# Kernel optimization log

Hardware: AMD Instinct MI355X
Metric: run time of the kernel (lower is better)

The kernel has to match this reference:

```python
import jax, jax.numpy as jnp
import numpy as np

H = 1024      # hidden_size
E = 8         # num_experts
I = 1024      # moe_intermediate_size
SI = 2816     # shared_expert_intermediate_size
B, S = 2, 2048


def setup_inputs() -> dict:
    key = jax.random.key(0)
    ks = jax.random.split(key, 10)
    sc = lambda fan_in: 1.0 / np.sqrt(fan_in)
    return {
        "hidden_states": jax.random.normal(ks[0], (B, S, H), dtype=jnp.float32),
        "gate_w": jax.random.normal(ks[1], (E, H), dtype=jnp.float32) * sc(H),
        "wg": jax.random.normal(ks[2], (E, I, H), dtype=jnp.float32) * sc(H),   # gate_proj per expert
        "wu": jax.random.normal(ks[3], (E, I, H), dtype=jnp.float32) * sc(H),   # up_proj per expert
        "wd": jax.random.normal(ks[4], (E, H, I), dtype=jnp.float32) * sc(I),   # down_proj per expert
        "swg": jax.random.normal(ks[5], (SI, H), dtype=jnp.float32) * sc(H),    # shared gate_proj
        "swu": jax.random.normal(ks[6], (SI, H), dtype=jnp.float32) * sc(H),    # shared up_proj
        "swd": jax.random.normal(ks[7], (H, SI), dtype=jnp.float32) * sc(SI),   # shared down_proj
        "shared_gate_w": jax.random.normal(ks[8], (1, H), dtype=jnp.float32) * sc(H),
        "top_k": 2,
    }


def reference(hidden_states, gate_w, wg, wu, wd, swg, swu, swd, shared_gate_w, top_k):
    b, s, h = hidden_states.shape
    flat = hidden_states.reshape(-1, h)                      # [T,H]
    # router
    logits = flat @ gate_w.T                                 # [T,E]
    probs = jax.nn.softmax(logits, axis=-1)
    vals, idx = jax.lax.top_k(probs, top_k)                  # [T,K]
    vals = vals / jnp.sum(vals, axis=-1, keepdims=True)      # norm_topk_prob
    # combine weights scattered to full expert dim: [T,E]
    combine = jnp.sum(jax.nn.one_hot(idx, E, dtype=flat.dtype) * vals[..., None], axis=1)
    # dense per-expert SwiGLU FFN over all tokens, masked-combined (same math)
    g = jax.nn.silu(jnp.einsum("th,eih->eti", flat, wg))     # [E,T,I]
    u = jnp.einsum("th,eih->eti", flat, wu)
    eo = jnp.einsum("eti,ehi->eth", g * u, wd)               # [E,T,H]
    expert_out = jnp.einsum("te,eth->th", combine, eo)       # [T,H]
    # shared expert with sigmoid gate
    shared = (jax.nn.silu(flat @ swg.T) * (flat @ swu.T)) @ swd.T   # [T,H]
    sgate = jax.nn.sigmoid(flat @ shared_gate_w.T)           # [T,1]
    out = expert_out + sgate * shared
    return out.reshape(b, s, h)
```

## Files before the change

kernel.cpp:

```cpp
#include <hip/hip_runtime.h>
#include <stdint.h>

#define TT  4096
#define HD  1024
#define NE  8
#define ID  1024
#define SID 2816

typedef short s16x8 __attribute__((ext_vector_type(8)));
typedef float f32x4 __attribute__((ext_vector_type(4)));
typedef float f32x4v __attribute__((ext_vector_type(4)));
typedef unsigned short u16x4 __attribute__((ext_vector_type(4)));

__device__ __forceinline__ ushort f2bf(float f) {
  uint32_t u = __float_as_uint(f);
  u += 0x7FFFu + ((u >> 16) & 1u);
  return (ushort)(u >> 16);
}

__device__ __forceinline__ float bf2f(ushort u) {
  return __uint_as_float((uint32_t)u << 16);
}

__device__ __forceinline__ void gll16(const ushort* g, ushort* l) {
  __builtin_amdgcn_global_load_lds(
      (const __attribute__((address_space(1))) void*)g,
      (__attribute__((address_space(3))) void*)l, 16, 0, 0);
}

struct CvtArgs {
  const float* src[6];
  ushort* dst[6];
  int n[6];
};

__global__ __launch_bounds__(256) void cvt_all(CvtArgs a) {
  int t = blockIdx.y;
  int i = (blockIdx.x * 256 + threadIdx.x) * 4;
  if (i >= a.n[t]) return;
  f32x4v v = *(const f32x4v*)(a.src[t] + i);
  u16x4 o;
  o.x = f2bf(v.x); o.y = f2bf(v.y); o.z = f2bf(v.z); o.w = f2bf(v.w);
  *(u16x4*)(a.dst[t] + i) = o;
}

__global__ __launch_bounds__(256) void router_k(
    const float* __restrict__ X, const float* __restrict__ gw,
    const float* __restrict__ sgw, ushort* __restrict__ Xb,
    int* __restrict__ topki, float* __restrict__ topkw,
    float* __restrict__ sgate) {
  __shared__ float gwL[(NE + 1) * HD];
  #pragma unroll
  for (int i = 0; i < NE * HD / 1024; i++) {
    int idx = i * 1024 + threadIdx.x * 4;
    *(f32x4*)&gwL[idx] = *(const f32x4*)&gw[idx];
  }
  {
    int idx = threadIdx.x * 4;
    if (idx < HD) *(f32x4*)&gwL[NE * HD + idx] = *(const f32x4*)&sgw[idx];
  }
  __syncthreads();

  const int wave = threadIdx.x >> 6, lane = threadIdx.x & 63;
  #pragma unroll
  for (int tt = 0; tt < 4; tt++) {
    const int t = blockIdx.x * 16 + wave * 4 + tt;
    const float* x = X + (size_t)t * HD;
    float acc[NE + 1];
    #pragma unroll
    for (int e = 0; e <= NE; e++) acc[e] = 0.f;
    #pragma unroll
    for (int p = 0; p < HD / 256; p++) {
      const int k = p * 256 + lane * 4;
      f32x4 xv = *(const f32x4*)&x[k];
      u16x4 xb;
      xb.x = f2bf(xv.x); xb.y = f2bf(xv.y); xb.z = f2bf(xv.z); xb.w = f2bf(xv.w);
      *(u16x4*)&Xb[(size_t)t * HD + k] = xb;
      #pragma unroll
      for (int e = 0; e < NE; e++) {
        f32x4 g = *(const f32x4*)&gwL[e * HD + k];
        acc[e] += xv.x * g.x + xv.y * g.y + xv.z * g.z + xv.w * g.w;
      }
      f32x4 s = *(const f32x4*)&gwL[NE * HD + k];
      acc[NE] += xv.x * s.x + xv.y * s.y + xv.z * s.z + xv.w * s.w;
    }
    #pragma unroll
    for (int off = 32; off > 0; off >>= 1)
      #pragma unroll
      for (int e = 0; e <= NE; e++)
        acc[e] += __shfl_xor(acc[e], off, 64);
    if (lane == 0) {
      float m = acc[0];
      #pragma unroll
      for (int e = 1; e < NE; e++) m = fmaxf(m, acc[e]);
      float p[NE];
      #pragma unroll
      for (int e = 0; e < NE; e++) p[e] = __expf(acc[e] - m);
      int i1 = 0;
      #pragma unroll
      for (int e = 1; e < NE; e++) if (p[e] > p[i1]) i1 = e;
      int i2 = (i1 == 0) ? 1 : 0;
      #pragma unroll
      for (int e = 0; e < NE; e++) if (e != i1 && p[e] > p[i2]) i2 = e;
      float inv = 1.f / (p[i1] + p[i2]);
      topki[2 * t] = i1; topki[2 * t + 1] = i2;
      topkw[2 * t] = p[i1] * inv; topkw[2 * t + 1] = p[i2] * inv;
      sgate[t] = 1.f / (1.f + __expf(-acc[NE]));
    }
  }
}

__global__ __launch_bounds__(1024) void binning_k(
    const int* __restrict__ topki, const float* __restrict__ topkw,
    int* __restrict__ cnt, int* __restrict__ offs,
    int* __restrict__ tokmap, float* __restrict__ wmap,
    int* __restrict__ smap) {
  __shared__ int wc[16][NE];
  __shared__ int wbase[16][NE];
  const int tid = threadIdx.x;
  const int wave = tid >> 6, lane = tid & 63;
  const uint64_t ltmask = ((uint64_t)1 << lane) - 1;

  int wcnt[NE];
  #pragma unroll
  for (int e = 0; e < NE; e++) wcnt[e] = 0;
  int mye[8], myoff[8];
  #pragma unroll
  for (int it = 0; it < 8; it++) {
    int s = wave * 512 + it * 64 + lane;
    int e = topki[s];
    mye[it] = e;
    myoff[it] = 0;
    #pragma unroll
    for (int ee = 0; ee < NE; ee++) {
      uint64_t m = __ballot(e == ee);
      if (e == ee) myoff[it] = wcnt[ee] + __popcll(m & ltmask);
      wcnt[ee] += __popcll(m);
    }
  }
  if (lane == 0) {
    #pragma unroll
    for (int e = 0; e < NE; e++) wc[wave][e] = wcnt[e];
  }
  __syncthreads();
  if (tid == 0) {
    int o = 0;
    for (int e = 0; e < NE; e++) {
      offs[e] = o;
      int tot = 0;
      for (int w = 0; w < 16; w++) { wbase[w][e] = o + tot; tot += wc[w][e]; }
      cnt[e] = tot;
      o += tot;
    }
  }
  __syncthreads();
  #pragma unroll
  for (int it = 0; it < 8; it++) {
    int s = wave * 512 + it * 64 + lane;
    int e = mye[it];
    int pos = wbase[wave][e] + myoff[it];
    tokmap[pos] = s >> 1;
    wmap[pos] = topkw[s];
    smap[s] = pos;
  }
}

constexpr int BM = 128, BN = 128, BK = 32;

template <bool GATHER>
__device__ __forceinline__ void gu_core(
    const ushort* __restrict__ A, const ushort* __restrict__ Wg,
    const ushort* __restrict__ Wu, ushort* __restrict__ Hout,
    const int* __restrict__ tokmap, int cnt, int seg,
    int mb, int nb, int N, int K) {
  const int m0 = mb * BM;
  if (m0 >= cnt) return;
  const int n0 = nb * BN;

  __shared__ ushort lA[2][BM * BK];
  __shared__ ushort lBg[2][BN * BK];
  __shared__ ushort lBu[2][BN * BK];

  const int tid = threadIdx.x;
  const int wave = tid >> 6, lane = tid & 63;
  const int wm = (wave >> 1) * 64, wn = (wave & 1) * 64;

  const int ar0 = wave * 32 + (lane >> 2);
  const int ar1 = ar0 + 16;
  const int kc = ((lane & 3) ^ ((lane >> 3) & 3)) * 8;

  const ushort *a0p, *a1p;
  if (GATHER) {
    int m_ = m0 + ar0;
    int tk0 = (m_ < cnt) ? tokmap[seg + m_] : 0;
    m_ = m0 + ar1;
    int tk1 = (m_ < cnt) ? tokmap[seg + m_] : 0;
    a0p = A + (size_t)tk0 * K + kc;
    a1p = A + (size_t)tk1 * K + kc;
  } else {
    a0p = A + (size_t)(m0 + ar0) * K + kc;
    a1p = A + (size_t)(m0 + ar1) * K + kc;
  }
  const ushort* bg0 = Wg + (size_t)(n0 + ar0) * K + kc;
  const ushort* bg1 = Wg + (size_t)(n0 + ar1) * K + kc;
  const ushort* bu0 = Wu + (size_t)(n0 + ar0) * K + kc;
  const ushort* bu1 = Wu + (size_t)(n0 + ar1) * K + kc;

  f32x4 accG[4][4], accU[4][4];
  #pragma unroll
  for (int i = 0; i < 4; i++)
    #pragma unroll
    for (int j = 0; j < 4; j++) {
      accG[i][j] = f32x4{0.f, 0.f, 0.f, 0.f};
      accU[i][j] = f32x4{0.f, 0.f, 0.f, 0.f};
    }

  const int lr = lane & 15;
  const int lk = (((lane >> 4) ^ ((lr >> 1) & 3))) * 8;
  const int w32 = wave * 32;

  auto stage = [&](int b, int k0) {
    gll16(a0p + k0, &lA[b][w32 * BK]);
    gll16(a1p + k0, &lA[b][(w32 + 16) * BK]);
    gll16(bg0 + k0, &lBg[b][w32 * BK]);
    gll16(bg1 + k0, &lBg[b][(w32 + 16) * BK]);
    gll16(bu0 + k0, &lBu[b][w32 * BK]);
    gll16(bu1 + k0, &lBu[b][(w32 + 16) * BK]);
  };

  const int nt = K / BK;
  stage(0, 0);
  for (int t = 0; t < nt; t++) {
    const int cur = t & 1;
    if (t + 1 < nt) {
      stage(cur ^ 1, (t + 1) * BK);
      asm volatile("s_waitcnt vmcnt(6)" ::: "memory");
    } else {
      asm volatile("s_waitcnt vmcnt(0)" ::: "memory");
    }
    __builtin_amdgcn_s_barrier();

    s16x8 af[4], bgf[4], buf_[4];
    #pragma unroll
    for (int i = 0; i < 4; i++) {
      af[i]   = *(const s16x8*)&lA [cur][(wm + i * 16 + lr) * BK + lk];
      bgf[i]  = *(const s16x8*)&lBg[cur][(wn + i * 16 + lr) * BK + lk];
      buf_[i] = *(const s16x8*)&lBu[cur][(wn + i * 16 + lr) * BK + lk];
    }
    #pragma unroll
    for (int i = 0; i < 4; i++)
      #pragma unroll
      for (int j = 0; j < 4; j++) {
        accG[i][j] = __builtin_amdgcn_mfma_f32_16x16x32_bf16(af[i], bgf[j], accG[i][j], 0, 0, 0);
        accU[i][j] = __builtin_amdgcn_mfma_f32_16x16x32_bf16(af[i], buf_[j], accU[i][j], 0, 0, 0);
      }
    __builtin_amdgcn_s_barrier();
  }

  const int lrr = (lane >> 4) * 4;
  #pragma unroll
  for (int i = 0; i < 4; i++) {
    #pragma unroll
    for (int r = 0; r < 4; r++) {
      int m = wm + i * 16 + lrr + r;
      if (m0 + m < cnt) {
        size_t row = (size_t)(seg + m0 + m) * N;
        #pragma unroll
        for (int j = 0; j < 4; j++) {
          int c = n0 + wn + j * 16 + lr;
          float g = accG[i][j][r];
          float u = accU[i][j][r];
          float s = g / (1.f + __expf(-g));
          Hout[row + c] = f2bf(s * u);
        }
      }
    }
  }
}

__device__ __forceinline__ void dn_core(
    const ushort* __restrict__ A, const ushort* __restrict__ W,
    ushort* __restrict__ outB, int cnt, int seg,
    int mb, int nb, int N, int K) {
  const int m0 = mb * BM;
  if (m0 >= cnt) return;
  const int n0 = nb * BN;

  __shared__ ushort lA[2][BM * BK];
  __shared__ ushort lB[2][BN * BK];

  const int tid = threadIdx.x;
  const int wave = tid >> 6, lane = tid & 63;
  const int wm = (wave >> 1) * 64, wn = (wave & 1) * 64;

  const int ar0 = wave * 32 + (lane >> 2);
  const int ar1 = ar0 + 16;
  const int kc = ((lane & 3) ^ ((lane >> 3) & 3)) * 8;

  int r0 = m0 + ar0; if (r0 > cnt - 1) r0 = cnt - 1;
  int r1 = m0 + ar1; if (r1 > cnt - 1) r1 = cnt - 1;
  const ushort* a0p = A + (size_t)(seg + r0) * K + kc;
  const ushort* a1p = A + (size_t)(seg + r1) * K + kc;
  const ushort* b0 = W + (size_t)(n0 + ar0) * K + kc;
  const ushort* b1 = W + (size_t)(n0 + ar1) * K + kc;

  f32x4 acc[4][4];
  #pragma unroll
  for (int i = 0; i < 4; i++)
    #pragma unroll
    for (int j = 0; j < 4; j++) acc[i][j] = f32x4{0.f, 0.f, 0.f, 0.f};

  const int lr = lane & 15;
  const int lk = (((lane >> 4) ^ ((lr >> 1) & 3))) * 8;
  const int w32 = wave * 32;

  auto stage = [&](int b, int k0) {
    gll16(a0p + k0, &lA[b][w32 * BK]);
    gll16(a1p + k0, &lA[b][(w32 + 16) * BK]);
    gll16(b0 + k0, &lB[b][w32 * BK]);
    gll16(b1 + k0, &lB[b][(w32 + 16) * BK]);
  };

  const int nt = K / BK;
  stage(0, 0);
  for (int t = 0; t < nt; t++) {
    const int cur = t & 1;
    if (t + 1 < nt) {
      stage(cur ^ 1, (t + 1) * BK);
      asm volatile("s_waitcnt vmcnt(4)" ::: "memory");
    } else {
      asm volatile("s_waitcnt vmcnt(0)" ::: "memory");
    }
    __builtin_amdgcn_s_barrier();

    s16x8 af[4], bf[4];
    #pragma unroll
    for (int i = 0; i < 4; i++) {
      af[i] = *(const s16x8*)&lA[cur][(wm + i * 16 + lr) * BK + lk];
      bf[i] = *(const s16x8*)&lB[cur][(wn + i * 16 + lr) * BK + lk];
    }
    #pragma unroll
    for (int i = 0; i < 4; i++)
      #pragma unroll
      for (int j = 0; j < 4; j++)
        acc[i][j] = __builtin_amdgcn_mfma_f32_16x16x32_bf16(af[i], bf[j], acc[i][j], 0, 0, 0);
    __builtin_amdgcn_s_barrier();
  }

  const int lrr = (lane >> 4) * 4;
  #pragma unroll
  for (int i = 0; i < 4; i++) {
    #pragma unroll
    for (int r = 0; r < 4; r++) {
      int m = wm + i * 16 + lrr + r;
      if (m0 + m < cnt) {
        size_t row = (size_t)(seg + m0 + m) * N;
        #pragma unroll
        for (int j = 0; j < 4; j++) {
          int c = n0 + wn + j * 16 + lr;
          outB[row + c] = f2bf(acc[i][j][r]);
        }
      }
    }
  }
}

__global__ __launch_bounds__(256, 2) void gemm_gu_s(
    const ushort* __restrict__ A, const ushort* __restrict__ Wg,
    const ushort* __restrict__ Wu, ushort* __restrict__ H,
    int M, int N, int K) {
  int id = blockIdx.x;
  int x = id & 7, k = id >> 3;
  int mb = (x & 3) * 8 + (k & 7);
  int nb = (x >> 2) * 11 + (k >> 3);
  gu_core<false>(A, Wg, Wu, H, nullptr, M, 0, mb, nb, N, K);
}

__global__ __launch_bounds__(256, 2) void gemm_gu_r(
    const ushort* __restrict__ A, const ushort* __restrict__ Wg,
    const ushort* __restrict__ Wu, ushort* __restrict__ H,
    const int* __restrict__ tokmap, const int* __restrict__ cnts,
    const int* __restrict__ offs, int N, int K) {
  int e = blockIdx.x;
  gu_core<true>(A, Wg + (size_t)e * N * K, Wu + (size_t)e * N * K, H,
                tokmap, cnts[e], offs[e], blockIdx.y, blockIdx.z, N, K);
}

__global__ __launch_bounds__(256, 2) void gemm_dn_s(
    const ushort* __restrict__ A, const ushort* __restrict__ W,
    float* __restrict__ out, const float* __restrict__ sgate,
    int M, int N, int K) {
  int id = blockIdx.x;
  int x = id & 7, kk = id >> 3;
  int mb = x * 4 + (kk & 3);
  int nb = kk >> 2;
  const int m0 = mb * 128, n0 = nb * 64;

  __shared__ ushort lA[2][128 * 32];
  __shared__ ushort lB[2][64 * 32];

  const int tid = threadIdx.x;
  const int wave = tid >> 6, lane = tid & 63;
  const int wm = (wave >> 1) * 64, wn = (wave & 1) * 32;

  const int ar0 = wave * 32 + (lane >> 2);
  const int ar1 = ar0 + 16;
  const int br  = wave * 16 + (lane >> 2);
  const int kc = ((lane & 3) ^ ((lane >> 3) & 3)) * 8;

  const ushort* a0p = A + (size_t)(m0 + ar0) * K + kc;
  const ushort* a1p = A + (size_t)(m0 + ar1) * K + kc;
  const ushort* bp  = W + (size_t)(n0 + br) * K + kc;

  f32x4 acc[4][2];
  #pragma unroll
  for (int i = 0; i < 4; i++)
    #pragma unroll
    for (int j = 0; j < 2; j++) acc[i][j] = f32x4{0.f, 0.f, 0.f, 0.f};

  const int lr = lane & 15;
  const int lk = (((lane >> 4) ^ ((lr >> 1) & 3))) * 8;
  const int w32 = wave * 32;

  auto stage = [&](int b, int k0) {
    gll16(a0p + k0, &lA[b][w32 * 32]);
    gll16(a1p + k0, &lA[b][(w32 + 16) * 32]);
    gll16(bp + k0, &lB[b][wave * 512]);
  };

  const int nt = K / 32;
  stage(0, 0);
  for (int t = 0; t < nt; t++) {
    const int cur = t & 1;
    if (t + 1 < nt) {
      stage(cur ^ 1, (t + 1) * 32);
      asm volatile("s_waitcnt vmcnt(3)" ::: "memory");
    } else {
      asm volatile("s_waitcnt vmcnt(0)" ::: "memory");
    }
    __builtin_amdgcn_s_barrier();

    s16x8 af[4], bf[2];
    #pragma unroll
    for (int i = 0; i < 4; i++)
      af[i] = *(const s16x8*)&lA[cur][(wm + i * 16 + lr) * 32 + lk];
    #pragma unroll
    for (int j = 0; j < 2; j++)
      bf[j] = *(const s16x8*)&lB[cur][(wn + j * 16 + lr) * 32 + lk];
    #pragma unroll
    for (int i = 0; i < 4; i++)
      #pragma unroll
      for (int j = 0; j < 2; j++)
        acc[i][j] = __builtin_amdgcn_mfma_f32_16x16x32_bf16(af[i], bf[j], acc[i][j], 0, 0, 0);
    __builtin_amdgcn_s_barrier();
  }

  const int lrr = (lane >> 4) * 4;
  #pragma unroll
  for (int i = 0; i < 4; i++) {
    #pragma unroll
    for (int r = 0; r < 4; r++) {
      int m = m0 + wm + i * 16 + lrr + r;
      float wv = sgate[m];
      size_t row = (size_t)m * N;
      #pragma unroll
      for (int j = 0; j < 2; j++) {
        int c = n0 + wn + j * 16 + lr;
        out[row + c] = wv * acc[i][j][r];
      }
    }
  }
}

__global__ __launch_bounds__(256, 2) void gemm_dn_r(
    const ushort* __restrict__ A, const ushort* __restrict__ W,
    ushort* __restrict__ eo, const int* __restrict__ cnts,
    const int* __restrict__ offs, int N, int K) {
  int e = blockIdx.x;
  dn_core(A, W + (size_t)e * N * K, eo, cnts[e], offs[e],
          blockIdx.y, blockIdx.z, N, K);
}

__global__ __launch_bounds__(256) void combine_k(
    const ushort* __restrict__ eo, const float* __restrict__ topkw,
    const int* __restrict__ smap, float* __restrict__ out) {
  int t = blockIdx.x;
  int c = threadIdx.x * 4;
  int s0 = smap[2 * t], s1 = smap[2 * t + 1];
  float w0 = topkw[2 * t], w1 = topkw[2 * t + 1];
  u16x4 a = *(const u16x4*)&eo[(size_t)s0 * HD + c];
  u16x4 b = *(const u16x4*)&eo[(size_t)s1 * HD + c];
  float* o = out + (size_t)t * HD + c;
  f32x4 ov = *(const f32x4*)o;
  #pragma unroll
  for (int j = 0; j < 4; j++)
    ov[j] += w0 * bf2f(a[j]) + w1 * bf2f(b[j]);
  *(f32x4*)o = ov;
}

extern "C" void kernel_launch(void* const* d_in, const int* in_sizes, int n_in,
                              void* d_out, int out_size, void* d_ws, size_t ws_size,
                              hipStream_t stream) {
  const float* hs  = (const float*)d_in[0];
  const float* gw  = (const float*)d_in[1];
  const float* wg  = (const float*)d_in[2];
  const float* wu  = (const float*)d_in[3];
  const float* wd  = (const float*)d_in[4];
  const float* swg = (const float*)d_in[5];
  const float* swu = (const float*)d_in[6];
  const float* swd = (const float*)d_in[7];
  const float* sgw = (const float*)d_in[8];
  float* out = (float*)d_out;

  uint8_t* base = (uint8_t*)d_ws;
  size_t off = 0;
  auto give = [&](size_t b) -> void* {
    void* p = base + off;
    off += (b + 255) & ~(size_t)255;
    return p;
  };
  ushort* Xb   = (ushort*)give((size_t)TT * HD * 2);
  ushort* wgB  = (ushort*)give((size_t)NE * ID * HD * 2);
  ushort* wuB  = (ushort*)give((size_t)NE * ID * HD * 2);
  ushort* wdB  = (ushort*)give((size_t)NE * HD * ID * 2);
  ushort* sgB  = (ushort*)give((size_t)SID * HD * 2);
  ushort* suB  = (ushort*)give((size_t)SID * HD * 2);
  ushort* sdB  = (ushort*)give((size_t)HD * SID * 2);
  ushort* Sbuf = (ushort*)give((size_t)TT * SID * 2);
  ushort* Hbuf = (ushort*)give((size_t)2 * TT * ID * 2);
  float* sgate = (float*)give(TT * 4);
  int* topki   = (int*)give(TT * 2 * 4);
  float* topkw = (float*)give(TT * 2 * 4);
  int* tokmap  = (int*)give(2 * TT * 4);
  float* wmap  = (float*)give(2 * TT * 4);
  int* smap    = (int*)give(2 * TT * 4);
  int* cnt     = (int*)give(256);
  int* offs    = (int*)give(256);

  CvtArgs ca;
  ca.src[0] = wg;  ca.dst[0] = wgB; ca.n[0] = NE * ID * HD;
  ca.src[1] = wu;  ca.dst[1] = wuB; ca.n[1] = NE * ID * HD;
  ca.src[2] = wd;  ca.dst[2] = wdB; ca.n[2] = NE * HD * ID;
  ca.src[3] = swg; ca.dst[3] = sgB; ca.n[3] = SID * HD;
  ca.src[4] = swu; ca.dst[4] = suB; ca.n[4] = SID * HD;
  ca.src[5] = swd; ca.dst[5] = sdB; ca.n[5] = HD * SID;
  cvt_all<<<dim3(8192, 6), 256, 0, stream>>>(ca);

  router_k<<<TT / 16, 256, 0, stream>>>(hs, gw, sgw, Xb, topki, topkw, sgate);
  binning_k<<<1, 1024, 0, stream>>>(topki, topkw, cnt, offs, tokmap, wmap, smap);

  gemm_gu_s<<<(TT / BM) * (SID / BN), 256, 0, stream>>>(
      Xb, sgB, suB, Sbuf, TT, SID, HD);
  gemm_dn_s<<<(TT / 128) * (HD / 64), 256, 0, stream>>>(
      Sbuf, sdB, out, sgate, TT, HD, SID);

  gemm_gu_r<<<dim3(NE, 2 * TT / BM, ID / BN), 256, 0, stream>>>(
      Xb, wgB, wuB, Hbuf, tokmap, cnt, offs, ID, HD);
  gemm_dn_r<<<dim3(NE, 2 * TT / BM, HD / BN), 256, 0, stream>>>(
      Hbuf, wdB, Sbuf , cnt, offs, HD, ID);

  combine_k<<<TT, 256, 0, stream>>>(Sbuf, topkw, smap, out);
}
```

Baseline: 276.4 us.

## Merge shared and routed expert GEMMs into combined launches with atomic combine

Shared-expert and routed-expert gate/up GEMMs now run in one launch, and the two down-projection GEMMs run in another, with blocks split by index. The routed down-projection scatters weighted results straight into the fp32 output with atomicAdd, which removes the bf16 intermediate buffer, the smap table and the separate combine kernel. The shared down-projection also uses atomicAdd, and the output is zeroed with a memset first. This cuts launches and tail idle time and fills the GPU with both workloads at once. In exchange it adds atomic traffic and makes the fp32 summation order nondeterministic. Many routed blocks (64 M-tiles per expert) exit early.

```diff
diff --git a/kernel.cpp b/kernel.cpp
--- a/kernel.cpp
+++ b/kernel.cpp
@@ -113,8 +113,7 @@
 __global__ __launch_bounds__(1024) void binning_k(
     const int* __restrict__ topki, const float* __restrict__ topkw,
     int* __restrict__ cnt, int* __restrict__ offs,
-    int* __restrict__ tokmap, float* __restrict__ wmap,
-    int* __restrict__ smap) {
+    int* __restrict__ tokmap, float* __restrict__ wmap) {
   __shared__ int wc[16][NE];
   __shared__ int wbase[16][NE];
   const int tid = threadIdx.x;
@@ -161,7 +160,6 @@
     int pos = wbase[wave][e] + myoff[it];
     tokmap[pos] = s >> 1;
     wmap[pos] = topkw[s];
-    smap[s] = pos;
   }
 }
 
@@ -172,14 +170,14 @@
     const ushort* __restrict__ A, const ushort* __restrict__ Wg,
     const ushort* __restrict__ Wu, ushort* __restrict__ Hout,
     const int* __restrict__ tokmap, int cnt, int seg,
-    int mb, int nb, int N, int K) {
+    int mb, int nb, int N, int K, ushort* lds) {
   const int m0 = mb * BM;
   if (m0 >= cnt) return;
   const int n0 = nb * BN;
 
-  __shared__ ushort lA[2][BM * BK];
-  __shared__ ushort lBg[2][BN * BK];
-  __shared__ ushort lBu[2][BN * BK];
+  ushort* lA  = lds;
+  ushort* lBg = lds + 8192;
+  ushort* lBu = lds + 16384;
 
   const int tid = threadIdx.x;
   const int wave = tid >> 6, lane = tid & 63;
@@ -220,12 +218,12 @@
   const int w32 = wave * 32;
 
   auto stage = [&](int b, int k0) {
-    gll16(a0p + k0, &lA[b][w32 * BK]);
-    gll16(a1p + k0, &lA[b][(w32 + 16) * BK]);
-    gll16(bg0 + k0, &lBg[b][w32 * BK]);
-    gll16(bg1 + k0, &lBg[b][(w32 + 16) * BK]);
-    gll16(bu0 + k0, &lBu[b][w32 * BK]);
-    gll16(bu1 + k0, &lBu[b][(w32 + 16) * BK]);
+    gll16(a0p + k0, &lA[b * 4096 + w32 * BK]);
+    gll16(a1p + k0, &lA[b * 4096 + (w32 + 16) * BK]);
+    gll16(bg0 + k0, &lBg[b * 4096 + w32 * BK]);
+    gll16(bg1 + k0, &lBg[b * 4096 + (w32 + 16) * BK]);
+    gll16(bu0 + k0, &lBu[b * 4096 + w32 * BK]);
+    gll16(bu1 + k0, &lBu[b * 4096 + (w32 + 16) * BK]);
   };
 
   const int nt = K / BK;
@@ -243,9 +241,9 @@
     s16x8 af[4], bgf[4], buf_[4];
     #pragma unroll
     for (int i = 0; i < 4; i++) {
-      af[i]   = *(const s16x8*)&lA [cur][(wm + i * 16 + lr) * BK + lk];
-      bgf[i]  = *(const s16x8*)&lBg[cur][(wn + i * 16 + lr) * BK + lk];
-      buf_[i] = *(const s16x8*)&lBu[cur][(wn + i * 16 + lr) * BK + lk];
+      af[i]   = *(const s16x8*)&lA [cur * 4096 + (wm + i * 16 + lr) * BK + lk];
+      bgf[i]  = *(const s16x8*)&lBg[cur * 4096 + (wn + i * 16 + lr) * BK + lk];
+      buf_[i] = *(const s16x8*)&lBu[cur * 4096 + (wn + i * 16 + lr) * BK + lk];
     }
     #pragma unroll
     for (int i = 0; i < 4; i++)
@@ -278,16 +276,17 @@
   }
 }
 
-__device__ __forceinline__ void dn_core(
+__device__ __forceinline__ void dn_r_core(
     const ushort* __restrict__ A, const ushort* __restrict__ W,
-    ushort* __restrict__ outB, int cnt, int seg,
-    int mb, int nb, int N, int K) {
+    float* __restrict__ out, const int* __restrict__ tokmap,
+    const float* __restrict__ wmap, int cnt, int seg,
+    int mb, int nb, int N, int K, ushort* lds) {
   const int m0 = mb * BM;
   if (m0 >= cnt) return;
   const int n0 = nb * BN;
 
-  __shared__ ushort lA[2][BM * BK];
-  __shared__ ushort lB[2][BN * BK];
+  ushort* lA = lds;
+  ushort* lB = lds + 8192;
 
   const int tid = threadIdx.x;
   const int wave = tid >> 6, lane = tid & 63;
@@ -315,10 +314,10 @@
   const int w32 = wave * 32;
 
   auto stage = [&](int b, int k0) {
-    gll16(a0p + k0, &lA[b][w32 * BK]);
-    gll16(a1p + k0, &lA[b][(w32 + 16) * BK]);
-    gll16(b0 + k0, &lB[b][w32 * BK]);
-    gll16(b1 + k0, &lB[b][(w32 + 16) * BK]);
+    gll16(a0p + k0, &lA[b * 4096 + w32 * BK]);
+    gll16(a1p + k0, &lA[b * 4096 + (w32 + 16) * BK]);
+    gll16(b0 + k0, &lB[b * 4096 + w32 * BK]);
+    gll16(b1 + k0, &lB[b * 4096 + (w32 + 16) * BK]);
   };
 
   const int nt = K / BK;
@@ -336,8 +335,8 @@
     s16x8 af[4], bf[4];
     #pragma unroll
     for (int i = 0; i < 4; i++) {
-      af[i] = *(const s16x8*)&lA[cur][(wm + i * 16 + lr) * BK + lk];
-      bf[i] = *(const s16x8*)&lB[cur][(wn + i * 16 + lr) * BK + lk];
+      af[i] = *(const s16x8*)&lA[cur * 4096 + (wm + i * 16 + lr) * BK + lk];
+      bf[i] = *(const s16x8*)&lB[cur * 4096 + (wn + i * 16 + lr) * BK + lk];
     }
     #pragma unroll
     for (int i = 0; i < 4; i++)
@@ -354,50 +353,28 @@
     for (int r = 0; r < 4; r++) {
       int m = wm + i * 16 + lrr + r;
       if (m0 + m < cnt) {
-        size_t row = (size_t)(seg + m0 + m) * N;
+        int slot = seg + m0 + m;
+        int t = tokmap[slot];
+        float wv = wmap[slot];
+        size_t row = (size_t)t * N;
         #pragma unroll
         for (int j = 0; j < 4; j++) {
           int c = n0 + wn + j * 16 + lr;
-          outB[row + c] = f2bf(acc[i][j][r]);
+          atomicAdd(&out[row + c], wv * acc[i][j][r]);
         }
       }
     }
   }
 }
 
-__global__ __launch_bounds__(256, 2) void gemm_gu_s(
-    const ushort* __restrict__ A, const ushort* __restrict__ Wg,
-    const ushort* __restrict__ Wu, ushort* __restrict__ H,
-    int M, int N, int K) {
-  int id = blockIdx.x;
-  int x = id & 7, k = id >> 3;
-  int mb = (x & 3) * 8 + (k & 7);
-  int nb = (x >> 2) * 11 + (k >> 3);
-  gu_core<false>(A, Wg, Wu, H, nullptr, M, 0, mb, nb, N, K);
-}
-
-__global__ __launch_bounds__(256, 2) void gemm_gu_r(
-    const ushort* __restrict__ A, const ushort* __restrict__ Wg,
-    const ushort* __restrict__ Wu, ushort* __restrict__ H,
-    const int* __restrict__ tokmap, const int* __restrict__ cnts,
-    const int* __restrict__ offs, int N, int K) {
-  int e = blockIdx.x;
-  gu_core<true>(A, Wg + (size_t)e * N * K, Wu + (size_t)e * N * K, H,
-                tokmap, cnts[e], offs[e], blockIdx.y, blockIdx.z, N, K);
-}
-
-__global__ __launch_bounds__(256, 2) void gemm_dn_s(
+__device__ __forceinline__ void dn_s_core(
     const ushort* __restrict__ A, const ushort* __restrict__ W,
     float* __restrict__ out, const float* __restrict__ sgate,
-    int M, int N, int K) {
-  int id = blockIdx.x;
-  int x = id & 7, kk = id >> 3;
-  int mb = x * 4 + (kk & 3);
-  int nb = kk >> 2;
+    int mb, int nb, int N, int K, ushort* lds) {
   const int m0 = mb * 128, n0 = nb * 64;
 
-  __shared__ ushort lA[2][128 * 32];
-  __shared__ ushort lB[2][64 * 32];
+  ushort* lA = lds;
+  ushort* lB = lds + 8192;
 
   const int tid = threadIdx.x;
   const int wave = tid >> 6, lane = tid & 63;
@@ -423,9 +400,9 @@
   const int w32 = wave * 32;
 
   auto stage = [&](int b, int k0) {
-    gll16(a0p + k0, &lA[b][w32 * 32]);
-    gll16(a1p + k0, &lA[b][(w32 + 16) * 32]);
-    gll16(bp + k0, &lB[b][wave * 512]);
+    gll16(a0p + k0, &lA[b * 4096 + w32 * 32]);
+    gll16(a1p + k0, &lA[b * 4096 + (w32 + 16) * 32]);
+    gll16(bp + k0, &lB[b * 2048 + wave * 512]);
   };
 
   const int nt = K / 32;
@@ -443,10 +420,10 @@
     s16x8 af[4], bf[2];
     #pragma unroll
     for (int i = 0; i < 4; i++)
-      af[i] = *(const s16x8*)&lA[cur][(wm + i * 16 + lr) * 32 + lk];
+      af[i] = *(const s16x8*)&lA[cur * 4096 + (wm + i * 16 + lr) * 32 + lk];
     #pragma unroll
     for (int j = 0; j < 2; j++)
-      bf[j] = *(const s16x8*)&lB[cur][(wn + j * 16 + lr) * 32 + lk];
+      bf[j] = *(const s16x8*)&lB[cur * 2048 + (wn + j * 16 + lr) * 32 + lk];
     #pragma unroll
     for (int i = 0; i < 4; i++)
       #pragma unroll
@@ -466,36 +443,57 @@
       #pragma unroll
       for (int j = 0; j < 2; j++) {
         int c = n0 + wn + j * 16 + lr;
-        out[row + c] = wv * acc[i][j][r];
+        atomicAdd(&out[row + c], wv * acc[i][j][r]);
       }
     }
   }
 }
 
-__global__ __launch_bounds__(256, 2) void gemm_dn_r(
-    const ushort* __restrict__ A, const ushort* __restrict__ W,
-    ushort* __restrict__ eo, const int* __restrict__ cnts,
-    const int* __restrict__ offs, int N, int K) {
-  int e = blockIdx.x;
-  dn_core(A, W + (size_t)e * N * K, eo, cnts[e], offs[e],
-          blockIdx.y, blockIdx.z, N, K);
-}
-
-__global__ __launch_bounds__(256) void combine_k(
-    const ushort* __restrict__ eo, const float* __restrict__ topkw,
-    const int* __restrict__ smap, float* __restrict__ out) {
-  int t = blockIdx.x;
-  int c = threadIdx.x * 4;
-  int s0 = smap[2 * t], s1 = smap[2 * t + 1];
-  float w0 = topkw[2 * t], w1 = topkw[2 * t + 1];
-  u16x4 a = *(const u16x4*)&eo[(size_t)s0 * HD + c];
-  u16x4 b = *(const u16x4*)&eo[(size_t)s1 * HD + c];
-  float* o = out + (size_t)t * HD + c;
-  f32x4 ov = *(const f32x4*)o;
-  #pragma unroll
-  for (int j = 0; j < 4; j++)
-    ov[j] += w0 * bf2f(a[j]) + w1 * bf2f(b[j]);
-  *(f32x4*)o = ov;
+#define GU_SH_BLKS 704
+__global__ __launch_bounds__(256, 2) void gemm_gu_m(
+    const ushort* __restrict__ Xb,
+    const ushort* __restrict__ sgB, const ushort* __restrict__ suB,
+    const ushort* __restrict__ wgB, const ushort* __restrict__ wuB,
+    ushort* __restrict__ Sbuf, ushort* __restrict__ Hbuf,
+    const int* __restrict__ tokmap, const int* __restrict__ cnts,
+    const int* __restrict__ offs) {
+  __shared__ ushort lds[24576];
+  int id = blockIdx.x;
+  if (id < GU_SH_BLKS) {
+    int x = id & 7, k = id >> 3;
+    int mb = (x & 3) * 8 + (k & 7);
+    int nb = (x >> 2) * 11 + (k >> 3);
+    gu_core<false>(Xb, sgB, suB, Sbuf, nullptr, TT, 0, mb, nb, SID, HD, lds);
+  } else {
+    int rid = id - GU_SH_BLKS;
+    int e = rid & 7, k = rid >> 3;
+    int mb = k >> 3, nb = k & 7;
+    gu_core<true>(Xb, wgB + (size_t)e * ID * HD, wuB + (size_t)e * ID * HD,
+                  Hbuf, tokmap, cnts[e], offs[e], mb, nb, ID, HD, lds);
+  }
+}
+
+#define DN_SH_BLKS 512
+__global__ __launch_bounds__(256, 2) void gemm_dn_m(
+    const ushort* __restrict__ Sbuf, const ushort* __restrict__ sdB,
+    const ushort* __restrict__ Hbuf, const ushort* __restrict__ wdB,
+    float* __restrict__ out, const float* __restrict__ sgate,
+    const int* __restrict__ tokmap, const float* __restrict__ wmap,
+    const int* __restrict__ cnts, const int* __restrict__ offs) {
+  __shared__ ushort lds[16384];
+  int id = blockIdx.x;
+  if (id < DN_SH_BLKS) {
+    int x = id & 7, kk = id >> 3;
+    int mb = x * 4 + (kk & 3);
+    int nb = kk >> 2;
+    dn_s_core(Sbuf, sdB, out, sgate, mb, nb, HD, SID, lds);
+  } else {
+    int rid = id - DN_SH_BLKS;
+    int e = rid & 7, k = rid >> 3;
+    int mb = k >> 3, nb = k & 7;
+    dn_r_core(Hbuf, wdB + (size_t)e * HD * ID, out, tokmap, wmap,
+              cnts[e], offs[e], mb, nb, HD, ID, lds);
+  }
 }
 
 extern "C" void kernel_launch(void* const* d_in, const int* in_sizes, int n_in,
@@ -533,9 +531,10 @@
   float* topkw = (float*)give(TT * 2 * 4);
   int* tokmap  = (int*)give(2 * TT * 4);
   float* wmap  = (float*)give(2 * TT * 4);
-  int* smap    = (int*)give(2 * TT * 4);
   int* cnt     = (int*)give(256);
   int* offs    = (int*)give(256);
+
+  hipMemsetAsync(out, 0, (size_t)out_size * 4, stream);
 
   CvtArgs ca;
   ca.src[0] = wg;  ca.dst[0] = wgB; ca.n[0] = NE * ID * HD;
@@ -547,17 +546,11 @@
   cvt_all<<<dim3(8192, 6), 256, 0, stream>>>(ca);
 
   router_k<<<TT / 16, 256, 0, stream>>>(hs, gw, sgw, Xb, topki, topkw, sgate);
-  binning_k<<<1, 1024, 0, stream>>>(topki, topkw, cnt, offs, tokmap, wmap, smap);
-
-  gemm_gu_s<<<(TT / BM) * (SID / BN), 256, 0, stream>>>(
-      Xb, sgB, suB, Sbuf, TT, SID, HD);
-  gemm_dn_s<<<(TT / 128) * (HD / 64), 256, 0, stream>>>(
-      Sbuf, sdB, out, sgate, TT, HD, SID);
-
-  gemm_gu_r<<<dim3(NE, 2 * TT / BM, ID / BN), 256, 0, stream>>>(
-      Xb, wgB, wuB, Hbuf, tokmap, cnt, offs, ID, HD);
-  gemm_dn_r<<<dim3(NE, 2 * TT / BM, HD / BN), 256, 0, stream>>>(
-      Hbuf, wdB, Sbuf , cnt, offs, HD, ID);
-
-  combine_k<<<TT, 256, 0, stream>>>(Sbuf, topkw, smap, out);
-}
+  binning_k<<<1, 1024, 0, stream>>>(topki, topkw, cnt, offs, tokmap, wmap);
+
+  gemm_gu_m<<<GU_SH_BLKS + NE * 64 * 8, 256, 0, stream>>>(
+      Xb, sgB, suB, wgB, wuB, Sbuf, Hbuf, tokmap, cnt, offs);
+
+  gemm_dn_m<<<DN_SH_BLKS + NE * 64 * 8, 256, 0, stream>>>(
+      Sbuf, sdB, Hbuf, wdB, out, sgate, tokmap, wmap, cnt, offs);
+}
```

New measurement: 244.5 us. -11.5%, faster.
